# Optimization experiments

Hardware: AMD Instinct MI355X
Metric: run time of the kernel (lower is better)

## Reference

```python
import jax, jax.numpy as jnp
import numpy as np

B, C, H, W = 1, 320, 64, 64
HEADS, DH = 8, 40            # inner_dim = 320
CTX_LEN, CTX_DIM = 77, 768
FF_MULT = 4
GN_GROUPS, GN_EPS = 32, 1e-6
LN_EPS = 1e-5
SCALE = DH ** -0.5
WSTD = 0.02


def setup_inputs() -> dict:
    key = jax.random.key(0)
    ks = iter(jax.random.split(key, 32))
    rn = lambda *s: jax.random.normal(next(ks), s, dtype=jnp.float32)
    D = HEADS * DH  # 320
    inp = {
        'hidden_states': rn(B, C, H, W),
        'encoder_hidden_states': rn(B, CTX_LEN, CTX_DIM),
        'gn_g': jnp.ones((C,), jnp.float32), 'gn_b': jnp.zeros((C,), jnp.float32),
        'pi_w': rn(C, D) * WSTD, 'pi_b': jnp.zeros((D,), jnp.float32),
        'n1_g': jnp.ones((D,), jnp.float32), 'n1_b': jnp.zeros((D,), jnp.float32),
        'a1_q': rn(D, D) * WSTD, 'a1_k': rn(D, D) * WSTD, 'a1_v': rn(D, D) * WSTD,
        'a1_o': rn(D, D) * WSTD, 'a1_ob': jnp.zeros((D,), jnp.float32),
        'n2_g': jnp.ones((D,), jnp.float32), 'n2_b': jnp.zeros((D,), jnp.float32),
        'a2_q': rn(D, D) * WSTD, 'a2_k': rn(CTX_DIM, D) * WSTD, 'a2_v': rn(CTX_DIM, D) * WSTD,
        'a2_o': rn(D, D) * WSTD, 'a2_ob': jnp.zeros((D,), jnp.float32),
        'n3_g': jnp.ones((D,), jnp.float32), 'n3_b': jnp.zeros((D,), jnp.float32),
        'ff_w1': rn(D, 2 * FF_MULT * D) * WSTD, 'ff_b1': jnp.zeros((2 * FF_MULT * D,), jnp.float32),
        'ff_w2': rn(FF_MULT * D, D) * WSTD, 'ff_b2': jnp.zeros((D,), jnp.float32),
        'po_w': rn(D, C) * WSTD, 'po_b': jnp.zeros((C,), jnp.float32),
    }
    return inp


def _group_norm(x, g, b):
    # x: [B,C,H,W]
    Bx, Cx, Hx, Wx = x.shape
    xr = x.reshape(Bx, GN_GROUPS, Cx // GN_GROUPS, Hx, Wx)
    mu = xr.mean(axis=(2, 3, 4), keepdims=True)
    var = xr.var(axis=(2, 3, 4), keepdims=True)
    xr = (xr - mu) * jax.lax.rsqrt(var + GN_EPS)
    x = xr.reshape(Bx, Cx, Hx, Wx)
    return x * g[None, :, None, None] + b[None, :, None, None]


def _layer_norm(x, g, b):
    mu = x.mean(-1, keepdims=True)
    var = x.var(-1, keepdims=True)
    return (x - mu) * jax.lax.rsqrt(var + LN_EPS) * g + b


def _attention(x, ctx, wq, wk, wv, wo, bo):
    # x: [B,S,D]; ctx: [B,T,Dc]. Same math as the torch sliced loop
    # (the 2-row slicing changes only execution order, not values).
    Bx, S, D = x.shape
    q = (x @ wq).reshape(Bx, S, HEADS, DH)
    k = (ctx @ wk).reshape(Bx, -1, HEADS, DH)
    v = (ctx @ wv).reshape(Bx, -1, HEADS, DH)
    s = jnp.einsum('bihd,bjhd->bhij', q, k) * SCALE
    p = jax.nn.softmax(s, axis=-1)
    o = jnp.einsum('bhij,bjhd->bihd', p, v).reshape(Bx, S, D)
    return o @ wo + bo


def reference(hidden_states, encoder_hidden_states, gn_g, gn_b, pi_w, pi_b,
              n1_g, n1_b, a1_q, a1_k, a1_v, a1_o, a1_ob,
              n2_g, n2_b, a2_q, a2_k, a2_v, a2_o, a2_ob,
              n3_g, n3_b, ff_w1, ff_b1, ff_w2, ff_b2, po_w, po_b):
    residual = hidden_states
    h = _group_norm(hidden_states, gn_g, gn_b)
    # proj_in: 1x1 conv == per-pixel linear; to [B, HW, D]
    h = jnp.einsum('bchw,cd->bhwd', h, pi_w) + pi_b
    Bx, Hx, Wx, D = h.shape
    h = h.reshape(Bx, Hx * Wx, D)

    # transformer block
    nh = _layer_norm(h, n1_g, n1_b)
    h = h + _attention(nh, nh, a1_q, a1_k, a1_v, a1_o, a1_ob)
    nh = _layer_norm(h, n2_g, n2_b)
    h = h + _attention(nh, encoder_hidden_states, a2_q, a2_k, a2_v, a2_o, a2_ob)
    nh = _layer_norm(h, n3_g, n3_b)
    hg = nh @ ff_w1 + ff_b1
    a, gate = jnp.split(hg, 2, axis=-1)  # GEGLU
    h = h + (a * jax.nn.gelu(gate, approximate=False)) @ ff_w2 + ff_b2

    # proj_out 1x1 conv then residual
    h = h.reshape(Bx, Hx, Wx, D)
    out = jnp.einsum('bhwd,dc->bchw', h, po_w) + po_b[None, :, None, None]
    return out + residual
```

## Files before the change

### kernel.cpp

```cpp
#include <hip/hip_runtime.h>

typedef __bf16 bf16x8 __attribute__((ext_vector_type(8)));
typedef __bf16 bf16x4 __attribute__((ext_vector_type(4)));
typedef __bf16 bf16x2 __attribute__((ext_vector_type(2)));
typedef float f32x4 __attribute__((ext_vector_type(4)));
typedef float f32x16 __attribute__((ext_vector_type(16)));

#define MFMA16(a, b, c) __builtin_amdgcn_mfma_f32_16x16x32_bf16(a, b, c, 0, 0, 0)
#define MFMA32(a, b, c) __builtin_amdgcn_mfma_f32_32x32x16_bf16(a, b, c, 0, 0, 0)

static constexpr float QSCALE = 0.15811388300841897f * 1.4426950408889634f;

__device__ __forceinline__ float fexp2(float x) { return __builtin_amdgcn_exp2f(x); }

__device__ __forceinline__ void gload16(const __bf16* g, __bf16* l) {
  __builtin_amdgcn_global_load_lds((const __attribute__((address_space(1))) void*)g,
                                   (__attribute__((address_space(3))) void*)l, 16, 0, 0);
}

__device__ __forceinline__ bf16x8 zero8() {
  bf16x8 z;
#pragma unroll
  for (int j = 0; j < 8; ++j) z[j] = (__bf16)0.0f;
  return z;
}

__device__ __forceinline__ bf16x8 ones8() {
  bf16x8 z;
#pragma unroll
  for (int j = 0; j < 8; ++j) z[j] = (__bf16)1.0f;
  return z;
}

__device__ __forceinline__ float gelu_exact(float x) {
  return 0.5f * x * (1.0f + erff(x * 0.70710678118654752f));
}

struct WDesc { const float* src; __bf16* dst; int K; int N; int ldn; int noff; };
struct WTable { WDesc w[12]; };

__global__ __launch_bounds__(256) void wconv_kernel(WTable tab) {
  WDesc d = tab.w[blockIdx.y];
  int total = (d.K >> 3) * d.N;
  int idx = blockIdx.x * 256 + threadIdx.x;
  if (idx >= total) return;
  int kb = idx / d.N, n = idx - kb * d.N;
  bf16x8 o;
#pragma unroll
  for (int j = 0; j < 8; ++j) o[j] = (__bf16)d.src[(size_t)(kb * 8 + j) * d.N + n];
  *(bf16x8*)&d.dst[((size_t)kb * d.ldn + d.noff + n) * 8] = o;
}

__global__ __launch_bounds__(256) void gn_stats(const float* __restrict__ X,
                                                float* __restrict__ part) {
  int g = blockIdx.x >> 3, cid = blockIdx.x & 7;
  const float* base = X + (size_t)g * 40960 + (size_t)cid * 5120;
  int t = threadIdx.x;
  float s = 0.f, s2 = 0.f;
#pragma unroll
  for (int i = t; i < 1280; i += 256) {
    float4 v = ((const float4*)base)[i];
    s += v.x + v.y + v.z + v.w;
    s2 += v.x * v.x + v.y * v.y + v.z * v.z + v.w * v.w;
  }
#pragma unroll
  for (int off = 1; off < 64; off <<= 1) { s += __shfl_xor(s, off); s2 += __shfl_xor(s2, off); }
  __shared__ float rs[4], rs2[4];
  int wid = t >> 6, lane = t & 63;
  if (lane == 0) { rs[wid] = s; rs2[wid] = s2; }
  __syncthreads();
  if (t == 0) {
    part[blockIdx.x * 2] = rs[0] + rs[1] + rs[2] + rs[3];
    part[blockIdx.x * 2 + 1] = rs2[0] + rs2[1] + rs2[2] + rs2[3];
  }
}

__global__ __launch_bounds__(256) void gn_apply(const float* __restrict__ X,
                                                const float* __restrict__ part,
                                                const float* __restrict__ gg,
                                                const float* __restrict__ gb,
                                                __bf16* __restrict__ Y) {
  int i0 = (blockIdx.x * 256 + threadIdx.x) * 8;
  int c = i0 >> 12, px = i0 & 4095;
  int g = c / 10;
  float s = 0.f, s2 = 0.f;
#pragma unroll
  for (int j = 0; j < 8; ++j) { s += part[(g * 8 + j) * 2]; s2 += part[(g * 8 + j) * 2 + 1]; }
  float mu = s * (1.f / 40960.f);
  float rstd = rsqrtf(s2 * (1.f / 40960.f) - mu * mu + 1e-6f);
  float ga = gg[c] * rstd, bb = gb[c] - mu * ga;
  float4 a = *(const float4*)&X[i0];
  float4 b = *(const float4*)&X[i0 + 4];
  Y[(size_t)(px + 0) * 320 + c] = (__bf16)(a.x * ga + bb);
  Y[(size_t)(px + 1) * 320 + c] = (__bf16)(a.y * ga + bb);
  Y[(size_t)(px + 2) * 320 + c] = (__bf16)(a.z * ga + bb);
  Y[(size_t)(px + 3) * 320 + c] = (__bf16)(a.w * ga + bb);
  Y[(size_t)(px + 4) * 320 + c] = (__bf16)(b.x * ga + bb);
  Y[(size_t)(px + 5) * 320 + c] = (__bf16)(b.y * ga + bb);
  Y[(size_t)(px + 6) * 320 + c] = (__bf16)(b.z * ga + bb);
  Y[(size_t)(px + 7) * 320 + c] = (__bf16)(b.w * ga + bb);
}

__global__ __launch_bounds__(256) void ln_kernel(const float* __restrict__ X,
                                                 const float* __restrict__ g,
                                                 const float* __restrict__ b,
                                                 __bf16* __restrict__ Y) {
  int row = blockIdx.x * 4 + (threadIdx.x >> 6);
  int lane = threadIdx.x & 63;
  const float* x = X + (size_t)row * 320;
  float v[5];
  float s = 0.f;
#pragma unroll
  for (int i = 0; i < 5; ++i) { v[i] = x[lane + 64 * i]; s += v[i]; }
#pragma unroll
  for (int off = 1; off < 64; off <<= 1) s += __shfl_xor(s, off);
  float mu = s * (1.f / 320.f);
  float s2 = 0.f;
#pragma unroll
  for (int i = 0; i < 5; ++i) { float d = v[i] - mu; s2 += d * d; }
#pragma unroll
  for (int off = 1; off < 64; off <<= 1) s2 += __shfl_xor(s2, off);
  float rstd = rsqrtf(s2 * (1.f / 320.f) + 1e-5f);
#pragma unroll
  for (int i = 0; i < 5; ++i) {
    int c = lane + 64 * i;
    Y[(size_t)row * 320 + c] = (__bf16)((v[i] - mu) * rstd * g[c] + b[c]);
  }
}

template <int OM, bool HB, bool HR, bool QS, bool AH>
__global__ __launch_bounds__(256) void gemm32(const __bf16* __restrict__ A,
                                              const __bf16* __restrict__ Bt,
                                              const float* __restrict__ bias,
                                              const float* __restrict__ res,
                                              void* __restrict__ Cout,
                                              void* __restrict__ Cout2,
                                              int M, int N, int K) {
  __shared__ __align__(16) __bf16 sA[2][2048];
  __shared__ __align__(16) __bf16 sB[2][4096];
  int t = threadIdx.x, lane = t & 63, wid = t >> 6;
  int wr = wid >> 1, wc = wid & 1, kb4 = lane >> 4, l15 = lane & 15;
  int id = blockIdx.x;
  int id2 = (id & 7) * 80 + (id >> 3);
  int bx = id2 / 5, by = id2 - bx * 5;
  int m0 = bx * 32, n0 = by * 64;
  const size_t N8 = (size_t)N * 8;
  f32x4 acc[2] = {};
  int r0 = t >> 3, c0 = (t & 7) ^ (r0 & 7);

  auto stage = [&](int buf, int k0) {
    const __bf16* ga0;
    if (AH) {
      int kk = k0 + c0 * 8;
      int hh = kk / 40, dh = kk - hh * 40;
      ga0 = &A[((size_t)hh * 4096 + m0 + r0) * 40 + dh];
    } else {
      ga0 = &A[(size_t)(m0 + r0) * K + k0 + c0 * 8];
    }
    gload16(ga0, &sA[buf][wid * 512]);
    gload16(&Bt[((size_t)(k0 >> 3) + wid) * N8 + (size_t)(n0 + lane) * 8], &sB[buf][wid * 512]);
    gload16(&Bt[((size_t)(k0 >> 3) + wid + 4) * N8 + (size_t)(n0 + lane) * 8], &sB[buf][2048 + wid * 512]);
  };
  stage(0, 0);
  __syncthreads();
  int cur = 0;
  for (int k0 = 0; k0 < K; k0 += 64) {
    if (k0 + 64 < K) stage(cur ^ 1, k0 + 64);
#pragma unroll
    for (int kk = 0; kk < 2; ++kk) {
      int c8 = kb4 + kk * 4;
      int row = wr * 16 + l15;
      bf16x8 af = *(const bf16x8*)&sA[cur][row * 64 + ((c8 * 8) ^ ((row & 7) << 3))];
      bf16x8 bfr[2];
#pragma unroll
      for (int fn = 0; fn < 2; ++fn)
        bfr[fn] = *(const bf16x8*)&sB[cur][(c8 * 64 + wc * 32 + fn * 16 + l15) * 8];
#pragma unroll
      for (int fn = 0; fn < 2; ++fn) acc[fn] = MFMA16(af, bfr[fn], acc[fn]);
    }
    __syncthreads();
    cur ^= 1;
  }
#pragma unroll
  for (int fn = 0; fn < 2; ++fn)
#pragma unroll
    for (int r = 0; r < 4; ++r) {
      int row = m0 + wr * 16 + kb4 * 4 + r;
      int col = n0 + wc * 32 + fn * 16 + l15;
      float v = acc[fn][r];
      if (HB) v += bias[col];
      if (OM == 3) {
        if (HR) v += res[(size_t)col * M + row];
        ((float*)Cout)[(size_t)col * M + row] = v;
      } else if (OM == 4) {
        int hh = col / 40, dh = col - hh * 40;
        __bf16* qp = (__bf16*)Cout + ((size_t)hh * 4096 + row) * 48 + dh;
        *qp = (__bf16)(QS ? v * QSCALE : v);
        if (dh >= 32) qp[8] = (__bf16)0.f;
      } else {
        if (HR) v += res[(size_t)row * N + col];
        if (OM == 0) {
          ((float*)Cout)[(size_t)row * N + col] = v;
        } else if (OM == 1) {
          ((__bf16*)Cout)[(size_t)row * N + col] = (__bf16)(QS ? v * QSCALE : v);
        } else {
          ((float*)Cout)[(size_t)row * N + col] = v;
          ((__bf16*)Cout2)[(size_t)row * N + col] = (__bf16)v;
        }
      }
    }
}

__device__ __forceinline__ void scatterK(__bf16* Kf, int NT, int hh, int row, int dh, float v) {
  int tile = row >> 6, kg = (row >> 5) & 1, k31 = row & 31;
  int s = dh >> 4, hi = (dh >> 3) & 1, j = dh & 7;
  size_t base = (((size_t)hh * NT + tile) * 2 + kg) * 3;
  Kf[(base + s) * 512 + (hi * 32 + k31) * 8 + j] = (__bf16)v;
  if (dh >= 32)
    Kf[(base + 2) * 512 + (32 + k31) * 8 + (dh & 7)] = (__bf16)0.f;
}
__device__ __forceinline__ void scatterV(__bf16* Vfl, __bf16* Vfh, int NT, int hh,
                                         int row, int dh, float v) {
  int tile = row >> 6, kg = (row >> 5) & 1, klo = row & 31;
  int m = (klo >> 4) & 1, hik = (klo >> 2) & 1;
  int jj = (klo & 3) | (((klo >> 3) & 1) << 2);
  size_t base = (((size_t)hh * NT + tile) * 2 + kg) * 2 + m;
  if (dh < 32) Vfl[base * 512 + (hik * 32 + dh) * 8 + jj] = (__bf16)v;
  else Vfh[base * 128 + (hik * 8 + (dh - 32)) * 8 + jj] = (__bf16)v;
}

__global__ __launch_bounds__(256) void qkv_gemm(const __bf16* __restrict__ A,
                                                const __bf16* __restrict__ Bt,
                                                __bf16* __restrict__ Qh,
                                                __bf16* __restrict__ Kf,
                                                __bf16* __restrict__ Vfl,
                                                __bf16* __restrict__ Vfh) {
  __shared__ __align__(16) __bf16 sA[2][4096];
  __shared__ __align__(16) __bf16 sB[2][4096];
  int t = threadIdx.x, lane = t & 63, wid = t >> 6;
  int wr = wid >> 1, wc = wid & 1, kb4 = lane >> 4, l15 = lane & 15;
  int id = blockIdx.x;
  int id2 = (id & 7) * 120 + (id >> 3);
  int bx = id2 / 15, by = id2 - bx * 15;
  int m0 = bx * 64, n0 = by * 64;
  f32x4 acc[2][2] = {};
  int r0 = t >> 3, c0 = (t & 7) ^ (r0 & 7);

  auto stage = [&](int buf, int k0) {
    gload16(&A[(size_t)(m0 + r0) * 320 + k0 + c0 * 8], &sA[buf][wid * 512]);
    gload16(&A[(size_t)(m0 + 32 + r0) * 320 + k0 + c0 * 8], &sA[buf][2048 + wid * 512]);
    gload16(&Bt[((size_t)(k0 >> 3) + wid) * (960 * 8) + (size_t)(n0 + lane) * 8], &sB[buf][wid * 512]);
    gload16(&Bt[((size_t)(k0 >> 3) + wid + 4) * (960 * 8) + (size_t)(n0 + lane) * 8], &sB[buf][2048 + wid * 512]);
  };
  stage(0, 0);
  __syncthreads();
  int cur = 0;
  for (int k0 = 0; k0 < 320; k0 += 64) {
    if (k0 + 64 < 320) stage(cur ^ 1, k0 + 64);
#pragma unroll
    for (int kk = 0; kk < 2; ++kk) {
      int c8 = kb4 + kk * 4;
      bf16x8 af[2], bfr[2];
#pragma unroll
      for (int fm = 0; fm < 2; ++fm) {
        int row = wr * 32 + fm * 16 + l15;
        af[fm] = *(const bf16x8*)&sA[cur][row * 64 + ((c8 * 8) ^ ((row & 7) << 3))];
      }
#pragma unroll
      for (int fn = 0; fn < 2; ++fn)
        bfr[fn] = *(const bf16x8*)&sB[cur][(c8 * 64 + wc * 32 + fn * 16 + l15) * 8];
#pragma unroll
      for (int fm = 0; fm < 2; ++fm)
#pragma unroll
        for (int fn = 0; fn < 2; ++fn) acc[fm][fn] = MFMA16(af[fm], bfr[fn], acc[fm][fn]);
    }
    __syncthreads();
    cur ^= 1;
  }
#pragma unroll
  for (int fm = 0; fm < 2; ++fm)
#pragma unroll
    for (int fn = 0; fn < 2; ++fn)
#pragma unroll
      for (int r = 0; r < 4; ++r) {
        int row = m0 + wr * 32 + fm * 16 + kb4 * 4 + r;
        int col = n0 + wc * 32 + fn * 16 + l15;
        float v = acc[fm][fn][r];
        if (col < 320) {
          int hh = col / 40, dh = col - hh * 40;
          __bf16* qp = &Qh[((size_t)hh * 4096 + row) * 48 + dh];
          *qp = (__bf16)(v * QSCALE);
          if (dh >= 32) qp[8] = (__bf16)0.f;
        } else if (col < 640) {
          int d = col - 320;
          int hh = d / 40, dh = d - hh * 40;
          scatterK(Kf, 64, hh, row, dh, v);
        } else {
          int d = col - 640;
          int hh = d / 40, dh = d - hh * 40;
          scatterV(Vfl, Vfh, 64, hh, row, dh, v);
        }
      }
}

__global__ __launch_bounds__(256) void kv2_gemm(const float* __restrict__ Af,
                                                const __bf16* __restrict__ Bt,
                                                __bf16* __restrict__ Kf,
                                                __bf16* __restrict__ Vfl,
                                                __bf16* __restrict__ Vfh) {
  __shared__ __align__(16) __bf16 sA[2][4][64][8];
  __shared__ __align__(16) __bf16 sB[2][4][64][8];
  int t = threadIdx.x, lane = t & 63, wid = t >> 6;
  int wr = wid >> 1, wc = wid & 1, kb4 = lane >> 4, l15 = lane & 15;
  int m0 = blockIdx.x * 64, n0 = blockIdx.y * 64;
  int am = t & 63, ac8 = t >> 6;
  int bn = t & 63, bkb = t >> 6;
  f32x4 acc[2][2] = {};
  bf16x8 rA, rB;
  auto loadA = [&](int k0) -> bf16x8 {
    if (m0 + am < 77) {
      const float* src = &Af[(size_t)(m0 + am) * 768 + k0 + ac8 * 8];
      float4 x = *(const float4*)src;
      float4 y = *(const float4*)(src + 4);
      bf16x8 o;
      o[0] = (__bf16)x.x; o[1] = (__bf16)x.y; o[2] = (__bf16)x.z; o[3] = (__bf16)x.w;
      o[4] = (__bf16)y.x; o[5] = (__bf16)y.y; o[6] = (__bf16)y.z; o[7] = (__bf16)y.w;
      return o;
    }
    return zero8();
  };
  auto loadB = [&](int k0) {
    return *(const bf16x8*)&Bt[((size_t)(k0 >> 3) + bkb) * (640 * 8) + (size_t)(n0 + bn) * 8];
  };
  rA = loadA(0); rB = loadB(0);
  *(bf16x8*)&sA[0][ac8][am][0] = rA;
  *(bf16x8*)&sB[0][bkb][bn][0] = rB;
  __syncthreads();
  int cur = 0;
  for (int k0 = 0; k0 < 768; k0 += 32, cur ^= 1) {
    bool more = (k0 + 32) < 768;
    if (more) { rA = loadA(k0 + 32); rB = loadB(k0 + 32); }
    bf16x8 af[2], bfr[2];
#pragma unroll
    for (int fm = 0; fm < 2; ++fm) af[fm] = *(const bf16x8*)&sA[cur][kb4][wr * 32 + fm * 16 + l15][0];
#pragma unroll
    for (int fn = 0; fn < 2; ++fn) bfr[fn] = *(const bf16x8*)&sB[cur][kb4][wc * 32 + fn * 16 + l15][0];
#pragma unroll
    for (int fm = 0; fm < 2; ++fm)
#pragma unroll
      for (int fn = 0; fn < 2; ++fn) acc[fm][fn] = MFMA16(af[fm], bfr[fn], acc[fm][fn]);
    if (more) {
      *(bf16x8*)&sA[cur ^ 1][ac8][am][0] = rA;
      *(bf16x8*)&sB[cur ^ 1][bkb][bn][0] = rB;
    }
    __syncthreads();
  }
#pragma unroll
  for (int fm = 0; fm < 2; ++fm)
#pragma unroll
    for (int fn = 0; fn < 2; ++fn)
#pragma unroll
      for (int r = 0; r < 4; ++r) {
        int row = m0 + wr * 32 + fm * 16 + kb4 * 4 + r;
        int col = n0 + wc * 32 + fn * 16 + l15;
        float v = acc[fm][fn][r];
        if (col < 320) {
          int hh = col / 40, dh = col - hh * 40;
          scatterK(Kf, 2, hh, row, dh, v);
        } else {
          int d = col - 320;
          int hh = d / 40, dh = d - hh * 40;
          scatterV(Vfl, Vfh, 2, hh, row, dh, v);
        }
      }
}

__global__ __launch_bounds__(256) void geglu64(const __bf16* __restrict__ A,
                                               const __bf16* __restrict__ Bt,
                                               const float* __restrict__ bias,
                                               __bf16* __restrict__ Out) {
  __shared__ __align__(16) __bf16 sA[2][4096];
  __shared__ __align__(16) __bf16 sB[2][4096];
  __shared__ __align__(16) __bf16 sBg[2][4096];
  int t = threadIdx.x, lane = t & 63, wid = t >> 6;
  int wr = wid >> 1, wc = wid & 1, kb4 = lane >> 4, l15 = lane & 15;
  int id = blockIdx.x;
  int id2 = (id & 7) * 160 + (id >> 3);
  int bx = id2 / 20, by = id2 - bx * 20;
  int m0 = bx * 64, n0 = by * 64;
  f32x4 acc_a[2][2] = {}, acc_g[2][2] = {};
  int r0 = t >> 3, c0 = (t & 7) ^ (r0 & 7);

  auto stage = [&](int buf, int k0) {
    gload16(&A[(size_t)(m0 + r0) * 320 + k0 + c0 * 8], &sA[buf][wid * 512]);
    gload16(&A[(size_t)(m0 + 32 + r0) * 320 + k0 + c0 * 8], &sA[buf][2048 + wid * 512]);
    gload16(&Bt[((size_t)(k0 >> 3) + wid) * (2560 * 8) + (size_t)(n0 + lane) * 8], &sB[buf][wid * 512]);
    gload16(&Bt[((size_t)(k0 >> 3) + wid + 4) * (2560 * 8) + (size_t)(n0 + lane) * 8], &sB[buf][2048 + wid * 512]);
    gload16(&Bt[((size_t)(k0 >> 3) + wid) * (2560 * 8) + (size_t)(1280 + n0 + lane) * 8], &sBg[buf][wid * 512]);
    gload16(&Bt[((size_t)(k0 >> 3) + wid + 4) * (2560 * 8) + (size_t)(1280 + n0 + lane) * 8], &sBg[buf][2048 + wid * 512]);
  };
  stage(0, 0);
  __syncthreads();
  int cur = 0;
  for (int k0 = 0; k0 < 320; k0 += 64) {
    if (k0 + 64 < 320) stage(cur ^ 1, k0 + 64);
#pragma unroll
    for (int kk = 0; kk < 2; ++kk) {
      int c8 = kb4 + kk * 4;
      bf16x8 af[2], bfa[2], bfg[2];
#pragma unroll
      for (int fm = 0; fm < 2; ++fm) {
        int row = wr * 32 + fm * 16 + l15;
        af[fm] = *(const bf16x8*)&sA[cur][row * 64 + ((c8 * 8) ^ ((row & 7) << 3))];
      }
#pragma unroll
      for (int fn = 0; fn < 2; ++fn) {
        bfa[fn] = *(const bf16x8*)&sB[cur][(c8 * 64 + wc * 32 + fn * 16 + l15) * 8];
        bfg[fn] = *(const bf16x8*)&sBg[cur][(c8 * 64 + wc * 32 + fn * 16 + l15) * 8];
      }
#pragma unroll
      for (int fm = 0; fm < 2; ++fm)
#pragma unroll
        for (int fn = 0; fn < 2; ++fn) {
          acc_a[fm][fn] = MFMA16(af[fm], bfa[fn], acc_a[fm][fn]);
          acc_g[fm][fn] = MFMA16(af[fm], bfg[fn], acc_g[fm][fn]);
        }
    }
    __syncthreads();
    cur ^= 1;
  }
#pragma unroll
  for (int fm = 0; fm < 2; ++fm)
#pragma unroll
    for (int fn = 0; fn < 2; ++fn)
#pragma unroll
      for (int r = 0; r < 4; ++r) {
        int row = m0 + wr * 32 + fm * 16 + kb4 * 4 + r;
        int col = n0 + wc * 32 + fn * 16 + l15;
        float a = acc_a[fm][fn][r] + bias[col];
        float g = acc_g[fm][fn][r] + bias[1280 + col];
        Out[(size_t)row * 1280 + col] = (__bf16)(a * gelu_exact(g));
      }
}

__global__ __launch_bounds__(512) void attn_kernel(const __bf16* __restrict__ Qh,
                                                   const __bf16* __restrict__ Kf,
                                                   const __bf16* __restrict__ Vfl,
                                                   const __bf16* __restrict__ Vfh,
                                                   __bf16* __restrict__ Oh,
                                                   int kv_len, int NT) {
  __shared__ float sO[9216];
  int t = threadIdx.x, lane = t & 63, wid = t >> 6;
  int zz = wid >> 2, kg = (wid >> 1) & 1, qg = wid & 1;
  int l31 = lane & 31, hi = lane >> 5;
  int id2 = ((blockIdx.x & 7) << 6) | (blockIdx.x >> 3);
  int h = id2 >> 6, q0 = (id2 & 63) * 64;
  int q = q0 + qg * 32 + l31;

  bf16x8 qf[3];
  {
    const __bf16* qrow = Qh + ((size_t)h * 4096 + q) * 48;
#pragma unroll
    for (int s = 0; s < 3; ++s) qf[s] = *(const bf16x8*)(qrow + s * 16 + hi * 8);
  }
  bf16x8 vfill = (l31 == 8) ? ones8() : zero8();
  f32x16 o_lo = {}, o_hi = {};

  int half = NT >> 1;
  int t0 = zz * half, t1 = t0 + half;
  for (int tile = t0; tile < t1; ++tile) {
    size_t kb = ((size_t)h * NT + tile) * 2 + kg;
    const __bf16* kp = Kf + kb * 3 * 512 + lane * 8;
    bf16x8 kf0 = *(const bf16x8*)(kp);
    bf16x8 kf1 = *(const bf16x8*)(kp + 512);
    bf16x8 kf2 = *(const bf16x8*)(kp + 1024);
    const __bf16* vp = Vfl + kb * 2 * 512 + lane * 8;
    bf16x8 vl0 = *(const bf16x8*)(vp);
    bf16x8 vl1 = *(const bf16x8*)(vp + 512);
    bf16x8 vh0 = vfill, vh1 = vfill;
    if (l31 < 8) {
      const __bf16* vph = Vfh + kb * 2 * 128 + (hi * 8 + l31) * 8;
      vh0 = *(const bf16x8*)(vph);
      vh1 = *(const bf16x8*)(vph + 128);
    }
    f32x16 s = {};
    __builtin_amdgcn_s_setprio(1);
    s = MFMA32(kf0, qf[0], s);
    s = MFMA32(kf1, qf[1], s);
    s = MFMA32(kf2, qf[2], s);
    __builtin_amdgcn_s_setprio(0);
    int k0 = tile << 6;
    if (k0 + 64 > kv_len) {
#pragma unroll
      for (int r = 0; r < 16; ++r) {
        int klo = (r & 3) + 8 * (r >> 2) + 4 * hi;
        if (k0 + kg * 32 + klo >= kv_len) s[r] = -1e30f;
      }
    }
    bf16x8 p0, p1;
#pragma unroll
    for (int j = 0; j < 8; ++j) {
      p0[j] = (__bf16)fexp2(s[j]);
      p1[j] = (__bf16)fexp2(s[8 + j]);
    }
    __builtin_amdgcn_s_setprio(1);
    o_lo = MFMA32(vl0, p0, o_lo);
    o_hi = MFMA32(vh0, p0, o_hi);
    o_lo = MFMA32(vl1, p1, o_lo);
    o_hi = MFMA32(vh1, p1, o_hi);
    __builtin_amdgcn_s_setprio(0);
  }
  int srcid = zz * 2 + kg;
  if (srcid != 0) {
    float* dst = sO + (((size_t)qg * 3 + (srcid - 1)) * 64 + lane) * 24;
#pragma unroll
    for (int r = 0; r < 16; ++r) dst[r] = o_lo[r];
#pragma unroll
    for (int r = 0; r < 4; ++r) dst[16 + r] = o_hi[r];
    dst[20] = o_hi[4];
  }
  __syncthreads();
  if (srcid == 0) {
#pragma unroll
    for (int src = 0; src < 3; ++src) {
      const float* sp = sO + (((size_t)qg * 3 + src) * 64 + lane) * 24;
#pragma unroll
      for (int r = 0; r < 16; ++r) o_lo[r] += sp[r];
#pragma unroll
      for (int r = 0; r < 4; ++r) o_hi[r] += sp[16 + r];
      o_hi[4] += sp[20];
    }
    float ls = __shfl(o_hi[4], l31);
    float inv = 1.0f / ls;
    __bf16* orow = Oh + ((size_t)h * 4096 + q) * 40;
#pragma unroll
    for (int r = 0; r < 16; r += 2) {
      int d = (r & 3) + 8 * (r >> 2) + 4 * hi;
      bf16x2 o2;
      o2[0] = (__bf16)(o_lo[r] * inv);
      o2[1] = (__bf16)(o_lo[r + 1] * inv);
      *(bf16x2*)(orow + d) = o2;
    }
#pragma unroll
    for (int r = 0; r < 4; r += 2) {
      int d = 32 + r + 4 * hi;
      bf16x2 o2;
      o2[0] = (__bf16)(o_hi[r] * inv);
      o2[1] = (__bf16)(o_hi[r + 1] * inv);
      *(bf16x2*)(orow + d) = o2;
    }
  }
}

extern "C" void kernel_launch(void* const* d_in, const int* in_sizes, int n_in,
                              void* d_out, int out_size, void* d_ws, size_t ws_size,
                              hipStream_t stream) {
  const float* hs    = (const float*)d_in[0];
  const float* ctx   = (const float*)d_in[1];
  const float* gn_g  = (const float*)d_in[2];
  const float* gn_b  = (const float*)d_in[3];
  const float* pi_w  = (const float*)d_in[4];
  const float* pi_b  = (const float*)d_in[5];
  const float* n1_g  = (const float*)d_in[6];
  const float* n1_b  = (const float*)d_in[7];
  const float* a1_q  = (const float*)d_in[8];
  const float* a1_k  = (const float*)d_in[9];
  const float* a1_v  = (const float*)d_in[10];
  const float* a1_o  = (const float*)d_in[11];
  const float* a1_ob = (const float*)d_in[12];
  const float* n2_g  = (const float*)d_in[13];
  const float* n2_b  = (const float*)d_in[14];
  const float* a2_q  = (const float*)d_in[15];
  const float* a2_k  = (const float*)d_in[16];
  const float* a2_v  = (const float*)d_in[17];
  const float* a2_o  = (const float*)d_in[18];
  const float* a2_ob = (const float*)d_in[19];
  const float* n3_g  = (const float*)d_in[20];
  const float* n3_b  = (const float*)d_in[21];
  const float* ff_w1 = (const float*)d_in[22];
  const float* ff_b1 = (const float*)d_in[23];
  const float* ff_w2 = (const float*)d_in[24];
  const float* ff_b2 = (const float*)d_in[25];
  const float* po_w  = (const float*)d_in[26];
  const float* po_b  = (const float*)d_in[27];

  char* p = (char*)d_ws;
  auto alloc = [&](size_t bytes) {
    char* r = p;
    p += (bytes + 255) & ~(size_t)255;
    return r;
  };
  __bf16* wPI  = (__bf16*)alloc((size_t)320 * 320 * 2);
  __bf16* wQKV = (__bf16*)alloc((size_t)320 * 960 * 2);
  __bf16* wO1  = (__bf16*)alloc((size_t)320 * 320 * 2);
  __bf16* wQ2  = (__bf16*)alloc((size_t)320 * 320 * 2);
  __bf16* wKV2 = (__bf16*)alloc((size_t)768 * 640 * 2);
  __bf16* wO2  = (__bf16*)alloc((size_t)320 * 320 * 2);
  __bf16* wFF1 = (__bf16*)alloc((size_t)320 * 2560 * 2);
  __bf16* wFF2 = (__bf16*)alloc((size_t)1280 * 320 * 2);
  __bf16* wPO  = (__bf16*)alloc((size_t)320 * 320 * 2);

  float*  gpart= (float*)alloc((size_t)256 * 2 * 4);
  __bf16* xg   = (__bf16*)alloc((size_t)4096 * 320 * 2);
  float*  h    = (float*)alloc((size_t)4096 * 320 * 4);
  __bf16* hb   = (__bf16*)alloc((size_t)4096 * 320 * 2);
  __bf16* nx   = (__bf16*)alloc((size_t)4096 * 320 * 2);
  __bf16* qh   = (__bf16*)alloc((size_t)8 * 4096 * 48 * 2);
  __bf16* kf   = (__bf16*)alloc((size_t)8 * 64 * 2 * 3 * 512 * 2);
  __bf16* vfl  = (__bf16*)alloc((size_t)8 * 64 * 2 * 2 * 512 * 2);
  __bf16* vfh  = (__bf16*)alloc((size_t)8 * 64 * 2 * 2 * 128 * 2);
  __bf16* kf2  = (__bf16*)alloc((size_t)8 * 2 * 2 * 3 * 512 * 2);
  __bf16* vfl2 = (__bf16*)alloc((size_t)8 * 2 * 2 * 2 * 512 * 2);
  __bf16* vfh2 = (__bf16*)alloc((size_t)8 * 2 * 2 * 2 * 128 * 2);
  __bf16* oh   = (__bf16*)alloc((size_t)4096 * 320 * 2);
  __bf16* g    = (__bf16*)alloc((size_t)4096 * 1280 * 2);
  float*  outp = (float*)d_out;

  WTable tab;
  tab.w[0]  = WDesc{pi_w,  wPI,  320, 320, 320, 0};
  tab.w[1]  = WDesc{a1_q,  wQKV, 320, 320, 960, 0};
  tab.w[2]  = WDesc{a1_k,  wQKV, 320, 320, 960, 320};
  tab.w[3]  = WDesc{a1_v,  wQKV, 320, 320, 960, 640};
  tab.w[4]  = WDesc{a1_o,  wO1,  320, 320, 320, 0};
  tab.w[5]  = WDesc{a2_q,  wQ2,  320, 320, 320, 0};
  tab.w[6]  = WDesc{a2_k,  wKV2, 768, 320, 640, 0};
  tab.w[7]  = WDesc{a2_v,  wKV2, 768, 320, 640, 320};
  tab.w[8]  = WDesc{a2_o,  wO2,  320, 320, 320, 0};
  tab.w[9]  = WDesc{ff_w1, wFF1, 320, 2560, 2560, 0};
  tab.w[10] = WDesc{ff_w2, wFF2, 1280, 320, 320, 0};
  tab.w[11] = WDesc{po_w,  wPO,  320, 320, 320, 0};
  wconv_kernel<<<dim3(400, 12), 256, 0, stream>>>(tab);
  gn_stats<<<dim3(256), 256, 0, stream>>>(hs, gpart);
  gn_apply<<<dim3(640), 256, 0, stream>>>(hs, gpart, gn_g, gn_b, xg);
  gemm32<0, true, false, false, false><<<dim3(640), 256, 0, stream>>>(xg, wPI, pi_b, nullptr, h, nullptr, 4096, 320, 320);
  ln_kernel<<<dim3(1024), 256, 0, stream>>>(h, n1_g, n1_b, nx);
  qkv_gemm<<<dim3(960), 256, 0, stream>>>(nx, wQKV, qh, kf, vfl, vfh);
  attn_kernel<<<dim3(512), 512, 0, stream>>>(qh, kf, vfl, vfh, oh, 4096, 64);
  gemm32<0, true, true, false, true><<<dim3(640), 256, 0, stream>>>(oh, wO1, a1_ob, h, h, nullptr, 4096, 320, 320);
  ln_kernel<<<dim3(1024), 256, 0, stream>>>(h, n2_g, n2_b, nx);
  gemm32<4, false, false, true, false><<<dim3(640), 256, 0, stream>>>(nx, wQ2, nullptr, nullptr, qh, nullptr, 4096, 320, 320);
  kv2_gemm<<<dim3(2, 10), 256, 0, stream>>>(ctx, wKV2, kf2, vfl2, vfh2);
  attn_kernel<<<dim3(512), 512, 0, stream>>>(qh, kf2, vfl2, vfh2, oh, 77, 2);
  gemm32<0, true, true, false, true><<<dim3(640), 256, 0, stream>>>(oh, wO2, a2_ob, h, h, nullptr, 4096, 320, 320);
  ln_kernel<<<dim3(1024), 256, 0, stream>>>(h, n3_g, n3_b, nx);
  geglu64<<<dim3(1280), 256, 0, stream>>>(nx, wFF1, ff_b1, g);
  gemm32<2, true, true, false, false><<<dim3(640), 256, 0, stream>>>(g, wFF2, ff_b2, h, h, hb, 4096, 320, 1280);
  gemm32<3, true, true, false, false><<<dim3(640), 256, 0, stream>>>(hb, wPO, po_b, hs, outp, nullptr, 4096, 320, 320);
}
```

Measured before the change: 164.8 us.

## Have each attention wave handle both query groups to reuse K/V fragments

Each wave in the attention kernel now processes both 32-query groups against the same K/V tiles, so every K and V fragment loaded from global memory feeds twice as many MFMAs. The KV range is split four ways across waves instead of two, and the partial results are combined by a two-stage reduction through a larger shared buffer. This aims to halve per-wave K/V global loads and raise MFMA density. In exchange it doubles the accumulator registers per wave, which may lower occupancy, and adds extra barriers and shared-memory traffic in the reduction.

```diff
diff --git a/kernel.cpp b/kernel.cpp
--- a/kernel.cpp
+++ b/kernel.cpp
@@ -449,105 +449,129 @@
                                                    const __bf16* __restrict__ Vfh,
                                                    __bf16* __restrict__ Oh,
                                                    int kv_len, int NT) {
-  __shared__ float sO[9216];
+  __shared__ float sO[12288];
   int t = threadIdx.x, lane = t & 63, wid = t >> 6;
-  int zz = wid >> 2, kg = (wid >> 1) & 1, qg = wid & 1;
+  int zz = wid >> 1, kg = wid & 1;
   int l31 = lane & 31, hi = lane >> 5;
   int id2 = ((blockIdx.x & 7) << 6) | (blockIdx.x >> 3);
   int h = id2 >> 6, q0 = (id2 & 63) * 64;
-  int q = q0 + qg * 32 + l31;
-
-  bf16x8 qf[3];
+
+  bf16x8 qf0[3], qf1[3];
   {
-    const __bf16* qrow = Qh + ((size_t)h * 4096 + q) * 48;
-#pragma unroll
-    for (int s = 0; s < 3; ++s) qf[s] = *(const bf16x8*)(qrow + s * 16 + hi * 8);
+    const __bf16* qr0 = Qh + ((size_t)h * 4096 + q0 + l31) * 48;
+    const __bf16* qr1 = Qh + ((size_t)h * 4096 + q0 + 32 + l31) * 48;
+#pragma unroll
+    for (int s = 0; s < 3; ++s) {
+      qf0[s] = *(const bf16x8*)(qr0 + s * 16 + hi * 8);
+      qf1[s] = *(const bf16x8*)(qr1 + s * 16 + hi * 8);
+    }
   }
   bf16x8 vfill = (l31 == 8) ? ones8() : zero8();
-  f32x16 o_lo = {}, o_hi = {};
-
-  int half = NT >> 1;
-  int t0 = zz * half, t1 = t0 + half;
+  f32x16 oL0 = {}, oH0 = {}, oL1 = {}, oH1 = {};
+
+  int half = (NT >= 4) ? (NT >> 2) : 1;
+  int t0 = zz * half; if (t0 > NT) t0 = NT;
+  int t1 = t0 + half; if (t1 > NT) t1 = NT;
   for (int tile = t0; tile < t1; ++tile) {
     size_t kb = ((size_t)h * NT + tile) * 2 + kg;
-    const __bf16* kp = Kf + kb * 3 * 512 + lane * 8;
+    const __bf16* kp = Kf + kb * 1536 + lane * 8;
     bf16x8 kf0 = *(const bf16x8*)(kp);
     bf16x8 kf1 = *(const bf16x8*)(kp + 512);
     bf16x8 kf2 = *(const bf16x8*)(kp + 1024);
-    const __bf16* vp = Vfl + kb * 2 * 512 + lane * 8;
+    const __bf16* vp = Vfl + kb * 1024 + lane * 8;
     bf16x8 vl0 = *(const bf16x8*)(vp);
     bf16x8 vl1 = *(const bf16x8*)(vp + 512);
     bf16x8 vh0 = vfill, vh1 = vfill;
     if (l31 < 8) {
-      const __bf16* vph = Vfh + kb * 2 * 128 + (hi * 8 + l31) * 8;
+      const __bf16* vph = Vfh + kb * 256 + (hi * 8 + l31) * 8;
       vh0 = *(const bf16x8*)(vph);
       vh1 = *(const bf16x8*)(vph + 128);
     }
-    f32x16 s = {};
+    f32x16 s0 = {}, s1 = {};
     __builtin_amdgcn_s_setprio(1);
-    s = MFMA32(kf0, qf[0], s);
-    s = MFMA32(kf1, qf[1], s);
-    s = MFMA32(kf2, qf[2], s);
+    s0 = MFMA32(kf0, qf0[0], s0);
+    s1 = MFMA32(kf0, qf1[0], s1);
+    s0 = MFMA32(kf1, qf0[1], s0);
+    s1 = MFMA32(kf1, qf1[1], s1);
+    s0 = MFMA32(kf2, qf0[2], s0);
+    s1 = MFMA32(kf2, qf1[2], s1);
     __builtin_amdgcn_s_setprio(0);
     int k0 = tile << 6;
     if (k0 + 64 > kv_len) {
 #pragma unroll
       for (int r = 0; r < 16; ++r) {
         int klo = (r & 3) + 8 * (r >> 2) + 4 * hi;
-        if (k0 + kg * 32 + klo >= kv_len) s[r] = -1e30f;
-      }
-    }
-    bf16x8 p0, p1;
+        if (k0 + kg * 32 + klo >= kv_len) { s0[r] = -1e30f; s1[r] = -1e30f; }
+      }
+    }
+    bf16x8 p00, p01, p10, p11;
 #pragma unroll
     for (int j = 0; j < 8; ++j) {
-      p0[j] = (__bf16)fexp2(s[j]);
-      p1[j] = (__bf16)fexp2(s[8 + j]);
+      p00[j] = (__bf16)fexp2(s0[j]);
+      p01[j] = (__bf16)fexp2(s0[8 + j]);
+      p10[j] = (__bf16)fexp2(s1[j]);
+      p11[j] = (__bf16)fexp2(s1[8 + j]);
     }
     __builtin_amdgcn_s_setprio(1);
-    o_lo = MFMA32(vl0, p0, o_lo);
-    o_hi = MFMA32(vh0, p0, o_hi);
-    o_lo = MFMA32(vl1, p1, o_lo);
-    o_hi = MFMA32(vh1, p1, o_hi);
+    oL0 = MFMA32(vl0, p00, oL0);
+    oL1 = MFMA32(vl0, p10, oL1);
+    oH0 = MFMA32(vh0, p00, oH0);
+    oH1 = MFMA32(vh0, p10, oH1);
+    oL0 = MFMA32(vl1, p01, oL0);
+    oL1 = MFMA32(vl1, p11, oL1);
+    oH0 = MFMA32(vh1, p01, oH0);
+    oH1 = MFMA32(vh1, p11, oH1);
     __builtin_amdgcn_s_setprio(0);
   }
   int srcid = zz * 2 + kg;
-  if (srcid != 0) {
-    float* dst = sO + (((size_t)qg * 3 + (srcid - 1)) * 64 + lane) * 24;
-#pragma unroll
-    for (int r = 0; r < 16; ++r) dst[r] = o_lo[r];
-#pragma unroll
-    for (int r = 0; r < 4; ++r) dst[16 + r] = o_hi[r];
-    dst[20] = o_hi[4];
-  }
+  auto dumpTo = [&](int slot, const f32x16& ol, const f32x16& oh, int qg) {
+    float* dst = sO + (((size_t)slot * 2 + qg) * 64 + lane) * 24;
+#pragma unroll
+    for (int r = 0; r < 16; ++r) dst[r] = ol[r];
+#pragma unroll
+    for (int r = 0; r < 4; ++r) dst[16 + r] = oh[r];
+    dst[20] = oh[4];
+  };
+  auto addFrom = [&](int slot, f32x16& ol, f32x16& oh, int qg) {
+    const float* sp = sO + (((size_t)slot * 2 + qg) * 64 + lane) * 24;
+#pragma unroll
+    for (int r = 0; r < 16; ++r) ol[r] += sp[r];
+#pragma unroll
+    for (int r = 0; r < 4; ++r) oh[r] += sp[16 + r];
+    oh[4] += sp[20];
+  };
+  if (srcid >= 4) { dumpTo(srcid - 4, oL0, oH0, 0); dumpTo(srcid - 4, oL1, oH1, 1); }
+  __syncthreads();
+  if (srcid < 4) { addFrom(srcid, oL0, oH0, 0); addFrom(srcid, oL1, oH1, 1); }
+  __syncthreads();
+  if (srcid >= 1 && srcid < 4) { dumpTo(srcid - 1, oL0, oH0, 0); dumpTo(srcid - 1, oL1, oH1, 1); }
   __syncthreads();
   if (srcid == 0) {
 #pragma unroll
-    for (int src = 0; src < 3; ++src) {
-      const float* sp = sO + (((size_t)qg * 3 + src) * 64 + lane) * 24;
-#pragma unroll
-      for (int r = 0; r < 16; ++r) o_lo[r] += sp[r];
-#pragma unroll
-      for (int r = 0; r < 4; ++r) o_hi[r] += sp[16 + r];
-      o_hi[4] += sp[20];
-    }
-    float ls = __shfl(o_hi[4], l31);
-    float inv = 1.0f / ls;
-    __bf16* orow = Oh + ((size_t)h * 4096 + q) * 40;
-#pragma unroll
-    for (int r = 0; r < 16; r += 2) {
-      int d = (r & 3) + 8 * (r >> 2) + 4 * hi;
-      bf16x2 o2;
-      o2[0] = (__bf16)(o_lo[r] * inv);
-      o2[1] = (__bf16)(o_lo[r + 1] * inv);
-      *(bf16x2*)(orow + d) = o2;
-    }
-#pragma unroll
-    for (int r = 0; r < 4; r += 2) {
-      int d = 32 + r + 4 * hi;
-      bf16x2 o2;
-      o2[0] = (__bf16)(o_hi[r] * inv);
-      o2[1] = (__bf16)(o_hi[r + 1] * inv);
-      *(bf16x2*)(orow + d) = o2;
+    for (int src = 0; src < 3; ++src) { addFrom(src, oL0, oH0, 0); addFrom(src, oL1, oH1, 1); }
+#pragma unroll
+    for (int qg = 0; qg < 2; ++qg) {
+      const f32x16& ol = qg ? oL1 : oL0;
+      const f32x16& oh = qg ? oH1 : oH0;
+      float ls = __shfl(oh[4], l31);
+      float inv = 1.0f / ls;
+      __bf16* orow = Oh + ((size_t)h * 4096 + q0 + qg * 32 + l31) * 40;
+#pragma unroll
+      for (int r = 0; r < 16; r += 2) {
+        int d = (r & 3) + 8 * (r >> 2) + 4 * hi;
+        bf16x2 o2;
+        o2[0] = (__bf16)(ol[r] * inv);
+        o2[1] = (__bf16)(ol[r + 1] * inv);
+        *(bf16x2*)(orow + d) = o2;
+      }
+#pragma unroll
+      for (int r = 0; r < 4; r += 2) {
+        int d = 32 + r + 4 * hi;
+        bf16x2 o2;
+        o2[0] = (__bf16)(oh[r] * inv);
+        o2[1] = (__bf16)(oh[r + 1] * inv);
+        *(bf16x2*)(orow + d) = o2;
+      }
     }
   }
 }
```

Result: no change. 165.5 us (+0.4%).
